# Kernel tuning notes

Hardware: AMD Instinct MI355X
Metric: run time of the kernel (lower is better)

Reference implementation:

```python
import jax, jax.numpy as jnp
import numpy as np

N = 524288
IN_C = 128
OUT_C = 256
GROUP = 8            # points per pooled cluster by construction (stride=2 -> code>>3)
K = N // GROUP       # number of pooled clusters (exact by construction)
POOLING_DEPTH = 1    # (ceil(stride=2)-1).bit_length() == 1, < serialized_depth
BN_EPS = 1e-3


def setup_inputs() -> dict:
    key = jax.random.key(0)
    k = jax.random.split(key, 8)
    feat = jax.random.normal(k[0], (N, IN_C), dtype=jnp.float32)
    coord = jax.random.normal(k[1], (N, 3), dtype=jnp.float32) * 50.0
    # 3 serialization orders; each is a permutation of arange(N) so code>>3 has
    # exactly K clusters of GROUP points each, with irregular membership.
    codes = [jax.random.permutation(k[2 + i], jnp.arange(N, dtype=jnp.int64)) for i in range(3)]
    serialized_code = jnp.stack(codes, axis=0)
    grid_coord = jax.random.randint(k[5], (N, 3), 0, 1024, dtype=jnp.int32)
    W = jax.random.normal(k[6], (OUT_C, IN_C), dtype=jnp.float32) / np.sqrt(IN_C).astype(np.float32)
    b = jnp.zeros((OUT_C,), jnp.float32)
    gamma = jnp.ones((OUT_C,), jnp.float32)
    beta = jnp.zeros((OUT_C,), jnp.float32)
    return {"feat": feat, "coord": coord, "W": W, "b": b, "gamma": gamma,
            "beta": beta, "serialized_code": serialized_code, "grid_coord": grid_coord}


def reference(feat, coord, W, b, gamma, beta, serialized_code, grid_coord):
    code = serialized_code >> (POOLING_DEPTH * 3)          # [3, N]
    code0 = code[0]
    # torch.unique(sorted=True, return_inverse, return_counts); K is static by construction
    _, cluster, counts = jnp.unique(code0, size=K, return_inverse=True, return_counts=True)
    indices = jnp.argsort(cluster)                          # group points by cluster
    idx_ptr = jnp.concatenate([jnp.zeros((1,), counts.dtype), jnp.cumsum(counts)])
    head_indices = indices[idx_ptr[:-1]]                    # first point of each cluster
    pooled_code = code[:, head_indices]                     # [3, K]
    pooled_order = jnp.argsort(pooled_code, axis=1)         # [3, K]
    # scatter_(1, order, arange) == argsort of the argsort
    pooled_inverse = jnp.argsort(pooled_order, axis=1)      # [3, K]
    # gather -> linear proj -> segment_csr max / mean over sorted groups
    projected = feat @ W.T + b                              # [N, OUT_C]
    seg_ids = cluster[indices]                              # sorted segment ids, [N]
    feat_max = jax.ops.segment_max(projected[indices], seg_ids, num_segments=K,
                                   indices_are_sorted=True)               # [K, OUT_C]
    coord_mean = jax.ops.segment_sum(coord[indices], seg_ids, num_segments=K,
                                     indices_are_sorted=True) / counts[:, None].astype(coord.dtype)
    # BatchNorm1d (training-mode batch stats, eps=1e-3) then exact GELU
    mean = jnp.mean(feat_max, axis=0)
    var = jnp.var(feat_max, axis=0)
    normed = (feat_max - mean) * jax.lax.rsqrt(var + BN_EPS) * gamma + beta
    out_feat = jax.nn.gelu(normed, approximate=False)       # [K, OUT_C]
    pooled_grid = grid_coord[head_indices] >> POOLING_DEPTH # [K, 3]
    return out_feat, coord_mean, pooled_code, pooled_order, pooled_inverse, pooled_grid
```

## Files before the change

kernel.cpp:

```cpp
#include <hip/hip_runtime.h>
#include <math.h>

#define N 524288
#define K 65536
#define IN_C 128
#define OUT_C 256

typedef __attribute__((ext_vector_type(8))) short short8;
typedef __attribute__((ext_vector_type(4))) float f32x4;

#define WS_INV     0
#define WS_CNT     2097152
#define WS_GPART   2621440
#define WS_CSUM    2752512
#define WS_ZLEN    1441792
#define WS_BLKSUM  3538944
#define WS_BINBUF  3540992
#define WS_WIMG    5638144
#define WS_MV      5703680
#define WS_FLAG    5705728

#define O_FEAT  0
#define O_CMEAN (K*256)
#define O_PCODE (O_CMEAN + K*3)
#define O_PORD  (O_PCODE + 3*K)
#define O_PINV  (O_PORD + 3*K)
#define O_PGRID (O_PINV + 3*K)

__device__ __forceinline__ int imin(int a, int b) { return a < b ? a : b; }

__device__ __forceinline__ unsigned short bf16_rne(float x) {
    unsigned int u = __float_as_uint(x);
    unsigned int r = u + 0x7fffu + ((u >> 16) & 1u);
    return (unsigned short)(r >> 16);
}

__global__ void wsplit_detect_kernel(const float* __restrict__ W, short* __restrict__ img,
                                     const unsigned int* __restrict__ sc, int* __restrict__ flag) {
    if (blockIdx.x == 16) {
        if (threadIdx.x < 64) {
            const unsigned int v = sc[threadIdx.x * 2 + 1];
            const unsigned long long b = __ballot(v != 0u);
            if (threadIdx.x == 0) *flag = (b != 0ull) ? 1 : 0;
        }
        return;
    }
    const int tid = blockIdx.x * 256 + threadIdx.x;
    const int col = tid >> 4;
    const int kc = tid & 15;
    const float4* wp = (const float4*)(W + col * IN_C + kc * 8);
    const float4 f0 = wp[0], f1 = wp[1];
    float xs[8] = {f0.x, f0.y, f0.z, f0.w, f1.x, f1.y, f1.z, f1.w};
    short8 hv;
#pragma unroll
    for (int j = 0; j < 8; ++j) hv[j] = (short)bf16_rne(xs[j]);
    *(short8*)&img[(col << 7) + ((kc ^ (col & 7)) << 3)] = hv;
}

__global__ void scatter_build_kernel(const void* __restrict__ sc, const int* __restrict__ flag,
                                     const float* __restrict__ coord,
                                     int* __restrict__ inv, float* __restrict__ csum) {
    const int i = blockIdx.x * 256 + threadIdx.x;
    long long v;
    if (*flag) v = (long long)((const int*)sc)[i];
    else       v = ((const long long*)sc)[i];
    const int vi = (int)v;
    inv[vi] = i;
    const int c = vi >> 3;
    const float* cp = coord + (size_t)i * 3;
    atomicAdd(&csum[c * 3 + 0], cp[0]);
    atomicAdd(&csum[c * 3 + 1], cp[1]);
    atomicAdd(&csum[c * 3 + 2], cp[2]);
}

#define SORT8(m, CSW) \
    CSW(m,0,1) CSW(m,2,3) CSW(m,4,5) CSW(m,6,7) \
    CSW(m,0,2) CSW(m,1,3) CSW(m,4,6) CSW(m,5,7) \
    CSW(m,1,2) CSW(m,5,6) \
    CSW(m,0,4) CSW(m,1,5) CSW(m,2,6) CSW(m,3,7) \
    CSW(m,2,4) CSW(m,3,5) \
    CSW(m,1,2) CSW(m,3,4) CSW(m,5,6)
#define CSWI(m,a,b) { int lo = imin(m[a], m[b]); int hi = (m[a] > m[b] ? m[a] : m[b]); m[a] = lo; m[b] = hi; }

__global__ void cluster_finish_kernel(const int* __restrict__ inv, const float* __restrict__ csum,
                                      const void* __restrict__ sc, const int* __restrict__ flag,
                                      const int* __restrict__ grid_coord,
                                      float* __restrict__ dout,
                                      int* __restrict__ cnt, unsigned short* __restrict__ binbuf) {
    const int c = blockIdx.x * 256 + threadIdx.x;
    int m[8];
#pragma unroll
    for (int j = 0; j < 8; ++j) m[j] = inv[c * 8 + j];
    int head = m[0];
#pragma unroll
    for (int j = 1; j < 8; ++j) head = imin(head, m[j]);

#pragma unroll
    for (int d = 0; d < 3; ++d) {
        dout[O_CMEAN + c * 3 + d] = csum[c * 3 + d] * 0.125f;
        dout[O_PGRID + c * 3 + d] = (float)(grid_coord[head * 3 + d] >> 1);
    }
    dout[O_PCODE + c] = (float)c;
    dout[O_PORD + c] = (float)c;
    dout[O_PINV + c] = (float)c;

    const int is32 = *flag;
#pragma unroll
    for (int r = 1; r < 3; ++r) {
        long long v = is32 ? (long long)((const int*)sc)[(size_t)r * N + head]
                           : ((const long long*)sc)[(size_t)r * N + head];
        const int pc = (int)(v >> 3);
        dout[O_PCODE + r * K + c] = (float)pc;
        const int idx = (r - 1) * K + pc;
        const int slot = atomicAdd(&cnt[idx], 1);
        binbuf[idx * 8 + slot] = (unsigned short)c;
    }
}

__global__ void scan1_kernel(const int* __restrict__ cnt, int* __restrict__ blksum) {
    __shared__ int lds[256];
    const int t = threadIdx.x;
    lds[t] = cnt[blockIdx.x * 256 + t];
    __syncthreads();
    for (int d = 128; d > 0; d >>= 1) { if (t < d) lds[t] += lds[t + d]; __syncthreads(); }
    if (t == 0) blksum[blockIdx.x] = lds[0];
}

__global__ void scan2_kernel(int* __restrict__ blksum) {
    __shared__ int lds[512];
    const int t = threadIdx.x;
    lds[t] = blksum[t];
    __syncthreads();
    for (int d = 1; d < 256; d <<= 1) {
        const int add = ((t & 255) >= d) ? lds[t - d] : 0;
        __syncthreads();
        lds[t] += add;
        __syncthreads();
    }
    blksum[t] = ((t & 255) == 0) ? 0 : lds[t - 1];
}

__global__ void scan3_kernel(const int* __restrict__ cnt, const int* __restrict__ blkbase,
                             int* __restrict__ base) {
    __shared__ int lds[256];
    const int t = threadIdx.x, gid = blockIdx.x * 256 + t;
    lds[t] = cnt[gid];
    __syncthreads();
    for (int d = 1; d < 256; d <<= 1) {
        const int add = (t >= d) ? lds[t - d] : 0;
        __syncthreads();
        lds[t] += add;
        __syncthreads();
    }
    base[gid] = blkbase[blockIdx.x] + ((t == 0) ? 0 : lds[t - 1]);
}

__global__ void scatter_kernel(const int* __restrict__ cnt, const int* __restrict__ base,
                               const unsigned short* __restrict__ binbuf, float* __restrict__ dout) {
    const int gid = blockIdx.x * 256 + threadIdx.x;
    const int n = cnt[gid];
    if (n == 0) return;
    int v[8];
#pragma unroll
    for (int j = 0; j < 8; ++j) v[j] = (j < n) ? (int)binbuf[gid * 8 + j] : 0x7fffffff;
    SORT8(v, CSWI)
    const int row = 1 + (gid >> 16);
    const int bp = base[gid];
#pragma unroll
    for (int j = 0; j < 8; ++j) {
        if (j < n) {
            const int cc = v[j];
            dout[O_PORD + row * K + bp + j] = (float)cc;
            dout[O_PINV + row * K + cc] = (float)(bp + j);
        }
    }
}

__global__ __launch_bounds__(512, 4) void gemm_max_kernel(
        const float* __restrict__ feat, const float4* __restrict__ wimg,
        const float* __restrict__ bias, const int* __restrict__ inv,
        float* __restrict__ out, float* __restrict__ gpart) {
    __shared__ short sWh[32768];
    __shared__ float bspart[512];
    const int t = threadIdx.x;
    const int blk = blockIdx.x;
    bspart[t] = 0.f;
    {
        float4* d = (float4*)sWh;
#pragma unroll
        for (int j = 0; j < 8; ++j) d[j * 512 + t] = wimg[j * 512 + t];
    }
    const int wid = t >> 6, l = t & 63;
    const int wr = wid >> 1, wc = wid & 1;
    const int lr = l & 15, lkg = l >> 4;

    const float* ap[2];
#pragma unroll
    for (int rt = 0; rt < 2; ++rt) {
        const int g = blk * 128 + wr * 32 + rt * 16 + lr;
        ap[rt] = feat + (size_t)inv[g] * IN_C + (lkg << 3);
    }

    f32x4 acc[2][8];
#pragma unroll
    for (int rt = 0; rt < 2; ++rt)
#pragma unroll
        for (int ct = 0; ct < 8; ++ct) acc[rt][ct] = (f32x4)0.f;

    __syncthreads();

#pragma unroll
    for (int ks = 0; ks < 4; ++ks) {
        short8 ah[2];
#pragma unroll
        for (int rt = 0; rt < 2; ++rt) {
            const float4 c0 = *(const float4*)(ap[rt] + ks * 32);
            const float4 c1 = *(const float4*)(ap[rt] + ks * 32 + 4);
            float xs[8] = {c0.x, c0.y, c0.z, c0.w, c1.x, c1.y, c1.z, c1.w};
#pragma unroll
            for (int j = 0; j < 8; ++j) ah[rt][j] = (short)bf16_rne(xs[j]);
        }
#pragma unroll
        for (int ct = 0; ct < 8; ++ct) {
            const int cc = wc * 128 + ct * 16 + lr;
            const int chunk = ((ks << 2) + lkg) ^ (cc & 7);
            const short8 bh = *(const short8*)&sWh[(cc << 7) + (chunk << 3)];
#pragma unroll
            for (int rt = 0; rt < 2; ++rt)
                acc[rt][ct] = __builtin_amdgcn_mfma_f32_16x16x32_bf16(ah[rt], bh, acc[rt][ct], 0, 0, 0);
        }
    }

    const int cb = blk * 16 + wr * 4;
    const bool valid = (l < 16) || (l >= 32 && l < 48);
    const int cg_add = (l >= 32) ? 1 : 0;
#pragma unroll
    for (int ct = 0; ct < 8; ++ct) {
        const int col = wc * 128 + ct * 16 + lr;
        const float bv = bias[col];
        float vb2[2];
#pragma unroll
        for (int rt = 0; rt < 2; ++rt) {
            const f32x4 a = acc[rt][ct];
            const float m4 = fmaxf(fmaxf(a[0], a[1]), fmaxf(a[2], a[3]));
            const float m8 = fmaxf(m4, __shfl_xor(m4, 16));
            vb2[rt] = m8 + bv;
            if (valid)
                out[O_FEAT + (size_t)(cb + rt * 2 + cg_add) * OUT_C + col] = vb2[rt];
        }
        float s = valid ? (vb2[0] + vb2[1]) : 0.f;
        float q = valid ? (vb2[0] * vb2[0] + vb2[1] * vb2[1]) : 0.f;
        s += __shfl_xor(s, 32);
        q += __shfl_xor(q, 32);
        if (l < 16) {
            atomicAdd(&bspart[col], s);
            atomicAdd(&bspart[256 + col], q);
        }
    }
    __syncthreads();
    atomicAdd(&gpart[(blk & 63) * 512 + t], bspart[t]);
}

__global__ void finalize_kernel(const float* __restrict__ gpart, float* __restrict__ mv) {
    __shared__ float sums[512];
    const int t = threadIdx.x;
    float s = 0.f;
    for (int j = 0; j < 64; ++j) s += gpart[j * 512 + t];
    sums[t] = s;
    __syncthreads();
    if (t < 256) {
        const float mean = sums[t] * (1.f / 65536.f);
        const float var = sums[256 + t] * (1.f / 65536.f) - mean * mean;
        mv[t] = mean;
        mv[256 + t] = rsqrtf(var + 0.001f);
    }
}

__global__ void bn_gelu_kernel(float* __restrict__ out, const float* __restrict__ mv,
                               const float* __restrict__ gamma, const float* __restrict__ beta) {
    const int gid = blockIdx.x * 256 + threadIdx.x;
    float4 v = ((float4*)out)[gid];
    const int o0 = (gid * 4) & 255;
    float r[4] = {v.x, v.y, v.z, v.w};
#pragma unroll
    for (int j = 0; j < 4; ++j) {
        const int o = o0 + j;
        float x = (r[j] - mv[o]) * mv[256 + o] * gamma[o] + beta[o];
        r[j] = x * 0.5f * (1.f + erff(x * 0.70710678118654752f));
    }
    ((float4*)out)[gid] = make_float4(r[0], r[1], r[2], r[3]);
}

extern "C" void kernel_launch(void* const* d_in, const int* in_sizes, int n_in,
                              void* d_out, int out_size, void* d_ws, size_t ws_size,
                              hipStream_t stream) {
    const float* feat  = (const float*)d_in[0];
    const float* coord = (const float*)d_in[1];
    const float* W     = (const float*)d_in[2];
    const float* bias  = (const float*)d_in[3];
    const float* gamma = (const float*)d_in[4];
    const float* beta  = (const float*)d_in[5];
    const void*  sc    = d_in[6];
    const int*   gridc = (const int*)d_in[7];
    float* out = (float*)d_out;
    char* ws = (char*)d_ws;

    int*   inv    = (int*)(ws + WS_INV);
    int*   cnt    = (int*)(ws + WS_CNT);
    float* gpart  = (float*)(ws + WS_GPART);
    float* csum   = (float*)(ws + WS_CSUM);
    int*   blksum = (int*)(ws + WS_BLKSUM);
    unsigned short* binbuf = (unsigned short*)(ws + WS_BINBUF);
    short* wimg   = (short*)(ws + WS_WIMG);
    float* mv     = (float*)(ws + WS_MV);
    int*   flag   = (int*)(ws + WS_FLAG);
    int*   base   = (int*)(ws + WS_INV);

    hipMemsetAsync(ws + WS_CNT, 0, WS_ZLEN, stream);
    wsplit_detect_kernel<<<17, 256, 0, stream>>>(W, wimg, (const unsigned int*)sc, flag);
    scatter_build_kernel<<<N / 256, 256, 0, stream>>>(sc, flag, coord, inv, csum);
    cluster_finish_kernel<<<K / 256, 256, 0, stream>>>(inv, csum, sc, flag, gridc, out, cnt, binbuf);
    gemm_max_kernel<<<N / 128, 512, 0, stream>>>(feat, (const float4*)wimg, bias, inv, out, gpart);
    scan1_kernel<<<512, 256, 0, stream>>>(cnt, blksum);
    scan2_kernel<<<1, 512, 0, stream>>>(blksum);
    scan3_kernel<<<512, 256, 0, stream>>>(cnt, blksum, base);
    scatter_kernel<<<512, 256, 0, stream>>>(cnt, base, binbuf, out);
    finalize_kernel<<<1, 512, 0, stream>>>(gpart, mv);
    bn_gelu_kernel<<<(K * 256) / (256 * 4), 256, 0, stream>>>(out, mv, gamma, beta);
}
```

Baseline: 625.1 us.

## Fuse prep and scan kernels, replace coord atomics, persist GEMM blocks with prefetch

Merges the weight conversion, flag detection, memset and inverse-scatter into one prep kernel. The coordinate atomics are replaced by a scatter of each point's coordinates into the output feature area, followed by a plain 8-way sum. The three-pass scan becomes a single-block scan, and the finalize step is folded into the scatter kernel. The GEMM now launches fewer, persistent blocks that loop over 8 tiles and software-prefetch the next tile's gathered rows. The goal is fewer launches, no atomic contention and better latency hiding, at the cost of a serial single-block scan and per-wave dtype detection by ballot.

```diff
diff --git a/kernel.cpp b/kernel.cpp
--- a/kernel.cpp
+++ b/kernel.cpp
@@ -12,13 +12,10 @@
 #define WS_INV     0
 #define WS_CNT     2097152
 #define WS_GPART   2621440
-#define WS_CSUM    2752512
-#define WS_ZLEN    1441792
-#define WS_BLKSUM  3538944
-#define WS_BINBUF  3540992
-#define WS_WIMG    5638144
-#define WS_MV      5703680
-#define WS_FLAG    5705728
+#define WS_BINBUF  2883584
+#define WS_WIMG    4980736
+#define WS_MV      5046272
+#define WS_FLAG    5048320
 
 #define O_FEAT  0
 #define O_CMEAN (K*256)
@@ -35,42 +32,42 @@
     return (unsigned short)(r >> 16);
 }
 
-__global__ void wsplit_detect_kernel(const float* __restrict__ W, short* __restrict__ img,
-                                     const unsigned int* __restrict__ sc, int* __restrict__ flag) {
-    if (blockIdx.x == 16) {
-        if (threadIdx.x < 64) {
-            const unsigned int v = sc[threadIdx.x * 2 + 1];
+__global__ void prep_kernel(const float* __restrict__ W, short* __restrict__ img,
+                            const void* __restrict__ sc, int* __restrict__ flag,
+                            const float* __restrict__ coord, int* __restrict__ inv,
+                            float* __restrict__ coordg,
+                            int* __restrict__ cnt, float* __restrict__ gpart) {
+    const int blk = blockIdx.x, t = threadIdx.x;
+    if (blk >= 2048) {
+        const int role = blk - 2048;
+        if (role < 16) {
+            const int tid = role * 256 + t;
+            const int col = tid >> 4;
+            const int kc = tid & 15;
+            const float4* wp = (const float4*)(W + col * IN_C + kc * 8);
+            const float4 f0 = wp[0], f1 = wp[1];
+            float xs[8] = {f0.x, f0.y, f0.z, f0.w, f1.x, f1.y, f1.z, f1.w};
+            short8 hv;
+#pragma unroll
+            for (int j = 0; j < 8; ++j) hv[j] = (short)bf16_rne(xs[j]);
+            *(short8*)&img[(col << 7) + ((kc ^ (col & 7)) << 3)] = hv;
+        } else if (t < 64) {
+            const unsigned int v = ((const unsigned int*)sc)[t * 2 + 1];
             const unsigned long long b = __ballot(v != 0u);
-            if (threadIdx.x == 0) *flag = (b != 0ull) ? 1 : 0;
+            if (t == 0) *flag = (b != 0ull) ? 1 : 0;
         }
         return;
     }
-    const int tid = blockIdx.x * 256 + threadIdx.x;
-    const int col = tid >> 4;
-    const int kc = tid & 15;
-    const float4* wp = (const float4*)(W + col * IN_C + kc * 8);
-    const float4 f0 = wp[0], f1 = wp[1];
-    float xs[8] = {f0.x, f0.y, f0.z, f0.w, f1.x, f1.y, f1.z, f1.w};
-    short8 hv;
-#pragma unroll
-    for (int j = 0; j < 8; ++j) hv[j] = (short)bf16_rne(xs[j]);
-    *(short8*)&img[(col << 7) + ((kc ^ (col & 7)) << 3)] = hv;
-}
-
-__global__ void scatter_build_kernel(const void* __restrict__ sc, const int* __restrict__ flag,
-                                     const float* __restrict__ coord,
-                                     int* __restrict__ inv, float* __restrict__ csum) {
-    const int i = blockIdx.x * 256 + threadIdx.x;
-    long long v;
-    if (*flag) v = (long long)((const int*)sc)[i];
-    else       v = ((const long long*)sc)[i];
-    const int vi = (int)v;
+    const int i = blk * 256 + t;
+    if (i < 2 * K) cnt[i] = 0;
+    if (i < 128 * 512) gpart[i] = 0.f;
+    const unsigned int hiw = ((const unsigned int*)sc)[2 * (size_t)i + 1];
+    const bool is32 = (__ballot(hiw != 0u) != 0ull);
+    const int vi = is32 ? ((const int*)sc)[i] : (int)((const long long*)sc)[i];
     inv[vi] = i;
-    const int c = vi >> 3;
     const float* cp = coord + (size_t)i * 3;
-    atomicAdd(&csum[c * 3 + 0], cp[0]);
-    atomicAdd(&csum[c * 3 + 1], cp[1]);
-    atomicAdd(&csum[c * 3 + 2], cp[2]);
+    float* cg = coordg + (size_t)vi * 3;
+    cg[0] = cp[0]; cg[1] = cp[1]; cg[2] = cp[2];
 }
 
 #define SORT8(m, CSW) \
@@ -82,7 +79,7 @@
     CSW(m,1,2) CSW(m,3,4) CSW(m,5,6)
 #define CSWI(m,a,b) { int lo = imin(m[a], m[b]); int hi = (m[a] > m[b] ? m[a] : m[b]); m[a] = lo; m[b] = hi; }
 
-__global__ void cluster_finish_kernel(const int* __restrict__ inv, const float* __restrict__ csum,
+__global__ void cluster_finish_kernel(const int* __restrict__ inv, const float* __restrict__ coordg,
                                       const void* __restrict__ sc, const int* __restrict__ flag,
                                       const int* __restrict__ grid_coord,
                                       float* __restrict__ dout,
@@ -95,11 +92,18 @@
 #pragma unroll
     for (int j = 1; j < 8; ++j) head = imin(head, m[j]);
 
-#pragma unroll
-    for (int d = 0; d < 3; ++d) {
-        dout[O_CMEAN + c * 3 + d] = csum[c * 3 + d] * 0.125f;
+    const float* cg = coordg + (size_t)c * 24;
+    float sx = 0.f, sy = 0.f, sz = 0.f;
+#pragma unroll
+    for (int j = 0; j < 8; ++j) { sx += cg[j * 3]; sy += cg[j * 3 + 1]; sz += cg[j * 3 + 2]; }
+    dout[O_CMEAN + c * 3 + 0] = sx * 0.125f;
+    dout[O_CMEAN + c * 3 + 1] = sy * 0.125f;
+    dout[O_CMEAN + c * 3 + 2] = sz * 0.125f;
+
+#pragma unroll
+    for (int d = 0; d < 3; ++d)
         dout[O_PGRID + c * 3 + d] = (float)(grid_coord[head * 3 + d] >> 1);
-    }
+
     dout[O_PCODE + c] = (float)c;
     dout[O_PORD + c] = (float)c;
     dout[O_PINV + c] = (float)c;
@@ -114,65 +118,6 @@
         const int idx = (r - 1) * K + pc;
         const int slot = atomicAdd(&cnt[idx], 1);
         binbuf[idx * 8 + slot] = (unsigned short)c;
-    }
-}
-
-__global__ void scan1_kernel(const int* __restrict__ cnt, int* __restrict__ blksum) {
-    __shared__ int lds[256];
-    const int t = threadIdx.x;
-    lds[t] = cnt[blockIdx.x * 256 + t];
-    __syncthreads();
-    for (int d = 128; d > 0; d >>= 1) { if (t < d) lds[t] += lds[t + d]; __syncthreads(); }
-    if (t == 0) blksum[blockIdx.x] = lds[0];
-}
-
-__global__ void scan2_kernel(int* __restrict__ blksum) {
-    __shared__ int lds[512];
-    const int t = threadIdx.x;
-    lds[t] = blksum[t];
-    __syncthreads();
-    for (int d = 1; d < 256; d <<= 1) {
-        const int add = ((t & 255) >= d) ? lds[t - d] : 0;
-        __syncthreads();
-        lds[t] += add;
-        __syncthreads();
-    }
-    blksum[t] = ((t & 255) == 0) ? 0 : lds[t - 1];
-}
-
-__global__ void scan3_kernel(const int* __restrict__ cnt, const int* __restrict__ blkbase,
-                             int* __restrict__ base) {
-    __shared__ int lds[256];
-    const int t = threadIdx.x, gid = blockIdx.x * 256 + t;
-    lds[t] = cnt[gid];
-    __syncthreads();
-    for (int d = 1; d < 256; d <<= 1) {
-        const int add = (t >= d) ? lds[t - d] : 0;
-        __syncthreads();
-        lds[t] += add;
-        __syncthreads();
-    }
-    base[gid] = blkbase[blockIdx.x] + ((t == 0) ? 0 : lds[t - 1]);
-}
-
-__global__ void scatter_kernel(const int* __restrict__ cnt, const int* __restrict__ base,
-                               const unsigned short* __restrict__ binbuf, float* __restrict__ dout) {
-    const int gid = blockIdx.x * 256 + threadIdx.x;
-    const int n = cnt[gid];
-    if (n == 0) return;
-    int v[8];
-#pragma unroll
-    for (int j = 0; j < 8; ++j) v[j] = (j < n) ? (int)binbuf[gid * 8 + j] : 0x7fffffff;
-    SORT8(v, CSWI)
-    const int row = 1 + (gid >> 16);
-    const int bp = base[gid];
-#pragma unroll
-    for (int j = 0; j < 8; ++j) {
-        if (j < n) {
-            const int cc = v[j];
-            dout[O_PORD + row * K + bp + j] = (float)cc;
-            dout[O_PINV + row * K + cc] = (float)(bp + j);
-        }
     }
 }
 
@@ -194,85 +139,172 @@
     const int wr = wid >> 1, wc = wid & 1;
     const int lr = l & 15, lkg = l >> 4;
 
-    const float* ap[2];
-#pragma unroll
-    for (int rt = 0; rt < 2; ++rt) {
-        const int g = blk * 128 + wr * 32 + rt * 16 + lr;
-        ap[rt] = feat + (size_t)inv[g] * IN_C + (lkg << 3);
-    }
-
-    f32x4 acc[2][8];
-#pragma unroll
-    for (int rt = 0; rt < 2; ++rt)
-#pragma unroll
-        for (int ct = 0; ct < 8; ++ct) acc[rt][ct] = (f32x4)0.f;
+    float bv[8];
+#pragma unroll
+    for (int ct = 0; ct < 8; ++ct) bv[ct] = bias[wc * 128 + ct * 16 + lr];
+
+    float sacc[8], qacc[8];
+#pragma unroll
+    for (int ct = 0; ct < 8; ++ct) { sacc[ct] = 0.f; qacc[ct] = 0.f; }
+
+    const int tile0 = blk * 8;
+    const float* ap;
+    {
+        const int iv = inv[tile0 * 64 + wr * 16 + lr];
+        ap = feat + (size_t)iv * IN_C + (lkg << 3);
+    }
+    float4 ra[4][2];
+#pragma unroll
+    for (int ks = 0; ks < 4; ++ks) {
+        ra[ks][0] = *(const float4*)(ap + ks * 32);
+        ra[ks][1] = *(const float4*)(ap + ks * 32 + 4);
+    }
 
     __syncthreads();
 
-#pragma unroll
-    for (int ks = 0; ks < 4; ++ks) {
-        short8 ah[2];
-#pragma unroll
-        for (int rt = 0; rt < 2; ++rt) {
-            const float4 c0 = *(const float4*)(ap[rt] + ks * 32);
-            const float4 c1 = *(const float4*)(ap[rt] + ks * 32 + 4);
-            float xs[8] = {c0.x, c0.y, c0.z, c0.w, c1.x, c1.y, c1.z, c1.w};
-#pragma unroll
-            for (int j = 0; j < 8; ++j) ah[rt][j] = (short)bf16_rne(xs[j]);
-        }
+#define CONV8(KS, AH) { \
+    const float4 c0 = ra[KS][0], c1 = ra[KS][1]; \
+    float xs[8] = {c0.x, c0.y, c0.z, c0.w, c1.x, c1.y, c1.z, c1.w}; \
+    _Pragma("unroll") \
+    for (int jj = 0; jj < 8; ++jj) AH[jj] = (short)bf16_rne(xs[jj]); }
+
+#define KSTEP(KS) { \
+    short8 ah; CONV8(KS, ah) \
+    _Pragma("unroll") \
+    for (int ct = 0; ct < 8; ++ct) { \
+        const int cc = wc * 128 + ct * 16 + lr; \
+        const int chunk = ((KS << 2) + lkg) ^ (cc & 7); \
+        const short8 bh = *(const short8*)&sWh[(cc << 7) + (chunk << 3)]; \
+        acc[ct] = __builtin_amdgcn_mfma_f32_16x16x32_bf16(ah, bh, acc[ct], 0, 0, 0); \
+    } }
+
+    for (int j = 0; j < 8; ++j) {
+        const int tile = tile0 + j;
+        int ivn = 0;
+        if (j < 7) ivn = inv[(tile + 1) * 64 + wr * 16 + lr];
+
+        f32x4 acc[8];
+#pragma unroll
+        for (int ct = 0; ct < 8; ++ct) acc[ct] = (f32x4)0.f;
+
+        const float* apn = ap;
+        KSTEP(0)
+        if (j < 7) {
+            apn = feat + (size_t)ivn * IN_C + (lkg << 3);
+            ra[0][0] = *(const float4*)(apn);
+            ra[0][1] = *(const float4*)(apn + 4);
+        }
+        KSTEP(1)
+        if (j < 7) {
+            ra[1][0] = *(const float4*)(apn + 32);
+            ra[1][1] = *(const float4*)(apn + 36);
+        }
+        KSTEP(2)
+        if (j < 7) {
+            ra[2][0] = *(const float4*)(apn + 64);
+            ra[2][1] = *(const float4*)(apn + 68);
+            ra[3][0] = *(const float4*)(apn + 96);
+            ra[3][1] = *(const float4*)(apn + 100);
+        }
+        KSTEP(3)
+
+        const int cb = tile * 8 + wr * 2;
+        const bool valid = (l < 16) || (l >= 32 && l < 48);
+        const int cg_add = (l >= 32) ? 1 : 0;
 #pragma unroll
         for (int ct = 0; ct < 8; ++ct) {
-            const int cc = wc * 128 + ct * 16 + lr;
-            const int chunk = ((ks << 2) + lkg) ^ (cc & 7);
-            const short8 bh = *(const short8*)&sWh[(cc << 7) + (chunk << 3)];
-#pragma unroll
-            for (int rt = 0; rt < 2; ++rt)
-                acc[rt][ct] = __builtin_amdgcn_mfma_f32_16x16x32_bf16(ah[rt], bh, acc[rt][ct], 0, 0, 0);
-        }
-    }
-
-    const int cb = blk * 16 + wr * 4;
-    const bool valid = (l < 16) || (l >= 32 && l < 48);
-    const int cg_add = (l >= 32) ? 1 : 0;
-#pragma unroll
-    for (int ct = 0; ct < 8; ++ct) {
-        const int col = wc * 128 + ct * 16 + lr;
-        const float bv = bias[col];
-        float vb2[2];
-#pragma unroll
-        for (int rt = 0; rt < 2; ++rt) {
-            const f32x4 a = acc[rt][ct];
+            const f32x4 a = acc[ct];
             const float m4 = fmaxf(fmaxf(a[0], a[1]), fmaxf(a[2], a[3]));
             const float m8 = fmaxf(m4, __shfl_xor(m4, 16));
-            vb2[rt] = m8 + bv;
+            const float vb = m8 + bv[ct];
             if (valid)
-                out[O_FEAT + (size_t)(cb + rt * 2 + cg_add) * OUT_C + col] = vb2[rt];
-        }
-        float s = valid ? (vb2[0] + vb2[1]) : 0.f;
-        float q = valid ? (vb2[0] * vb2[0] + vb2[1] * vb2[1]) : 0.f;
-        s += __shfl_xor(s, 32);
-        q += __shfl_xor(q, 32);
-        if (l < 16) {
-            atomicAdd(&bspart[col], s);
-            atomicAdd(&bspart[256 + col], q);
+                out[O_FEAT + (size_t)(cb + cg_add) * OUT_C + wc * 128 + ct * 16 + lr] = vb;
+            float s = valid ? vb : 0.f;
+            float q = valid ? vb * vb : 0.f;
+            s += __shfl_xor(s, 32);
+            q += __shfl_xor(q, 32);
+            sacc[ct] += s;
+            qacc[ct] += q;
+        }
+        ap = apn;
+    }
+
+    if (l < 16) {
+#pragma unroll
+        for (int ct = 0; ct < 8; ++ct) {
+            const int col = wc * 128 + ct * 16 + lr;
+            atomicAdd(&bspart[col], sacc[ct]);
+            atomicAdd(&bspart[256 + col], qacc[ct]);
         }
     }
     __syncthreads();
-    atomicAdd(&gpart[(blk & 63) * 512 + t], bspart[t]);
-}
-
-__global__ void finalize_kernel(const float* __restrict__ gpart, float* __restrict__ mv) {
+    atomicAdd(&gpart[(blk & 127) * 512 + t], bspart[t]);
+}
+
+__global__ void scan_fused_kernel(const int* __restrict__ cnt, int* __restrict__ base) {
+    __shared__ int lds[1024];
+    const int t = threadIdx.x;
+    const int4* cp = (const int4*)(cnt + t * 128);
+    int s = 0;
+#pragma unroll 8
+    for (int u = 0; u < 32; ++u) { const int4 v = cp[u]; s += v.x + v.y + v.z + v.w; }
+    lds[t] = s;
+    __syncthreads();
+    for (int d = 1; d < 1024; d <<= 1) {
+        const int a = (t >= d) ? lds[t - d] : 0;
+        __syncthreads();
+        lds[t] += a;
+        __syncthreads();
+    }
+    int off = ((t == 0) ? 0 : lds[t - 1]) - ((t >= 512) ? K : 0);
+    int4* bp = (int4*)(base + t * 128);
+#pragma unroll 8
+    for (int u = 0; u < 32; ++u) {
+        const int4 v = cp[u];
+        int4 w;
+        w.x = off; off += v.x;
+        w.y = off; off += v.y;
+        w.z = off; off += v.z;
+        w.w = off; off += v.w;
+        bp[u] = w;
+    }
+}
+
+__global__ void scatter_fin_kernel(const int* __restrict__ cnt, const int* __restrict__ base,
+                                   const unsigned short* __restrict__ binbuf,
+                                   float* __restrict__ dout,
+                                   const float* __restrict__ gpart, float* __restrict__ mv) {
     __shared__ float sums[512];
-    const int t = threadIdx.x;
-    float s = 0.f;
-    for (int j = 0; j < 64; ++j) s += gpart[j * 512 + t];
-    sums[t] = s;
-    __syncthreads();
-    if (t < 256) {
-        const float mean = sums[t] * (1.f / 65536.f);
-        const float var = sums[256 + t] * (1.f / 65536.f) - mean * mean;
-        mv[t] = mean;
-        mv[256 + t] = rsqrtf(var + 0.001f);
+    const int blk = blockIdx.x, t = threadIdx.x;
+    if (blk == 256) {
+        float s = 0.f;
+        for (int r = 0; r < 128; ++r) s += gpart[r * 512 + t];
+        sums[t] = s;
+        __syncthreads();
+        if (t < 256) {
+            const float mean = sums[t] * (1.f / 65536.f);
+            const float var = sums[256 + t] * (1.f / 65536.f) - mean * mean;
+            mv[t] = mean;
+            mv[256 + t] = rsqrtf(var + 0.001f);
+        }
+        return;
+    }
+    const int gid = blk * 512 + t;
+    const int n = cnt[gid];
+    if (n == 0) return;
+    int v[8];
+#pragma unroll
+    for (int j = 0; j < 8; ++j) v[j] = (j < n) ? (int)binbuf[gid * 8 + j] : 0x7fffffff;
+    SORT8(v, CSWI)
+    const int row = 1 + (gid >> 16);
+    const int bp = base[gid];
+#pragma unroll
+    for (int j = 0; j < 8; ++j) {
+        if (j < n) {
+            const int cc = v[j];
+            dout[O_PORD + row * K + bp + j] = (float)cc;
+            dout[O_PINV + row * K + cc] = (float)(bp + j);
+        }
     }
 }
 
@@ -308,23 +340,17 @@
     int*   inv    = (int*)(ws + WS_INV);
     int*   cnt    = (int*)(ws + WS_CNT);
     float* gpart  = (float*)(ws + WS_GPART);
-    float* csum   = (float*)(ws + WS_CSUM);
-    int*   blksum = (int*)(ws + WS_BLKSUM);
     unsigned short* binbuf = (unsigned short*)(ws + WS_BINBUF);
     short* wimg   = (short*)(ws + WS_WIMG);
     float* mv     = (float*)(ws + WS_MV);
     int*   flag   = (int*)(ws + WS_FLAG);
     int*   base   = (int*)(ws + WS_INV);
-
-    hipMemsetAsync(ws + WS_CNT, 0, WS_ZLEN, stream);
-    wsplit_detect_kernel<<<17, 256, 0, stream>>>(W, wimg, (const unsigned int*)sc, flag);
-    scatter_build_kernel<<<N / 256, 256, 0, stream>>>(sc, flag, coord, inv, csum);
-    cluster_finish_kernel<<<K / 256, 256, 0, stream>>>(inv, csum, sc, flag, gridc, out, cnt, binbuf);
-    gemm_max_kernel<<<N / 128, 512, 0, stream>>>(feat, (const float4*)wimg, bias, inv, out, gpart);
-    scan1_kernel<<<512, 256, 0, stream>>>(cnt, blksum);
-    scan2_kernel<<<1, 512, 0, stream>>>(blksum);
-    scan3_kernel<<<512, 256, 0, stream>>>(cnt, blksum, base);
-    scatter_kernel<<<512, 256, 0, stream>>>(cnt, base, binbuf, out);
-    finalize_kernel<<<1, 512, 0, stream>>>(gpart, mv);
+    float* coordg = out + O_FEAT;
+
+    prep_kernel<<<2065, 256, 0, stream>>>(W, wimg, sc, flag, coord, inv, coordg, cnt, gpart);
+    cluster_finish_kernel<<<K / 256, 256, 0, stream>>>(inv, coordg, sc, flag, gridc, out, cnt, binbuf);
+    gemm_max_kernel<<<1024, 512, 0, stream>>>(feat, (const float4*)wimg, bias, inv, out, gpart);
+    scan_fused_kernel<<<1, 1024, 0, stream>>>(cnt, base);
+    scatter_fin_kernel<<<257, 512, 0, stream>>>(cnt, base, binbuf, out, gpart, mv);
     bn_gelu_kernel<<<(K * 256) / (256 * 4), 256, 0, stream>>>(out, mv, gamma, beta);
 }
```

After: 824.1 us. 31.8% more time.
